# Kernel tuning notes

Hardware: AMD Instinct MI355X
Metric: run time of the kernel (lower is better)

## Reference

```python
import math
import jax, jax.numpy as jnp
import numpy as np

N_HEAD = 16
BLOCK_SIZE = 2048


def setup_inputs() -> dict:
    key = jax.random.key(0)
    ks = jax.random.split(key, 6)
    B, L, D = 2, 2048, 1024
    hs = D // N_HEAD
    s = 0.02
    return {
        "x": jax.random.normal(ks[0], (B, L, D), dtype=jnp.float32),
        "Wqkv": jax.random.normal(ks[1], (D, 3 * D), dtype=jnp.float32) * s,
        "bqkv": jax.random.normal(ks[2], (3 * D,), dtype=jnp.float32) * s,
        "Wproj": jax.random.normal(ks[3], (D, D), dtype=jnp.float32) * s,
        "bproj": jax.random.normal(ks[4], (D,), dtype=jnp.float32) * s,
        "Er": jax.random.normal(ks[5], (BLOCK_SIZE, hs), dtype=jnp.float32),
    }


def _skew(QEr):
    # QEr: [B, H, L, L] -> pad one zero column on the left, reshape, drop first row
    B, H, R, C = QEr.shape
    padded = jnp.pad(QEr, ((0, 0), (0, 0), (0, 0), (1, 0)))  # [B,H,R,C+1]
    reshaped = padded.reshape(B, H, C + 1, R)
    return reshaped[:, :, 1:, :]  # [B,H,R,C]


def reference(x, Wqkv, bqkv, Wproj, bproj, Er):
    B, L, D = x.shape
    H = N_HEAD
    hs = D // H
    qkv = x @ Wqkv + bqkv  # [B,L,3D]
    q, k, v = jnp.split(qkv, 3, axis=-1)
    q = q.reshape(B, L, H, hs).transpose(0, 2, 1, 3)  # [B,H,L,hs]
    k = k.reshape(B, L, H, hs).transpose(0, 2, 1, 3)
    v = v.reshape(B, L, H, hs).transpose(0, 2, 1, 3)

    Er_used = Er[BLOCK_SIZE - L:, :]           # [L, hs]
    QEr = jnp.einsum('bhld,md->bhlm', q, Er_used)  # q @ Er^T -> [B,H,L,L]
    Srel = _skew(QEr)

    scale = 1.0 / math.sqrt(hs)
    att = (jnp.einsum('bhld,bhmd->bhlm', q, k) + Srel) * scale
    causal = jnp.tril(jnp.ones((L, L), dtype=bool))
    att = jnp.where(causal[None, None], att, -jnp.inf)
    att = jax.nn.softmax(att, axis=-1)
    y = jnp.einsum('bhlm,bhmd->bhld', att, v)  # [B,H,L,hs]
    y = y.transpose(0, 2, 1, 3).reshape(B, L, D)
    return y @ Wproj + bproj
```

## Files before the change

kernel.cpp:

```cpp
#include <hip/hip_runtime.h>
#include <hip/hip_bf16.h>

#define LSEQ 2048
#define NH 16
#define HS 64
#define DIM 1024

typedef __attribute__((ext_vector_type(8))) short short8;
typedef __attribute__((ext_vector_type(4))) float f32x4;

typedef const __attribute__((address_space(1))) void g_void_t;
typedef __attribute__((address_space(3))) void s_void_t;

#define QSCALE 0.18033688011112042f

static __device__ __forceinline__ short f2bf(float f) {
  __hip_bfloat16 h = __float2bfloat16(f);
  return __builtin_bit_cast(short, h);
}

static __device__ __forceinline__ float fexp2(float x) {
#if __has_builtin(__builtin_amdgcn_exp2f)
  return __builtin_amdgcn_exp2f(x);
#else
  float r; asm("v_exp_f32 %0, %1" : "=v"(r) : "v"(x)); return r;
#endif
}

template<int CTRL>
static __device__ __forceinline__ float dpp_mov(float x) {
  return __builtin_bit_cast(float,
      __builtin_amdgcn_update_dpp(0, __builtin_bit_cast(int, x), CTRL, 0xF, 0xF, true));
}
static __device__ __forceinline__ float redmax16(float x) {
  x = fmaxf(x, dpp_mov<0xB1>(x));
  x = fmaxf(x, dpp_mov<0x4E>(x));
  x = fmaxf(x, dpp_mov<0x141>(x));
  x = fmaxf(x, dpp_mov<0x140>(x));
  return x;
}
static __device__ __forceinline__ float redsum16(float x) {
  x += dpp_mov<0xB1>(x);
  x += dpp_mov<0x4E>(x);
  x += dpp_mov<0x141>(x);
  x += dpp_mov<0x140>(x);
  return x;
}


__global__ void cast_kernel(const float* __restrict__ in, short* __restrict__ out, int n4) {
  int i = blockIdx.x * blockDim.x + threadIdx.x;
  if (i < n4) {
    float4 v = reinterpret_cast<const float4*>(in)[i];
    short4 o;
    o.x = f2bf(v.x); o.y = f2bf(v.y); o.z = f2bf(v.z); o.w = f2bf(v.w);
    reinterpret_cast<short4*>(out)[i] = o;
  }
}

__global__ void transpose_cast_kernel(const float* __restrict__ W, short* __restrict__ Wt,
                                      int K, int N) {
  __shared__ float tile[64][65];
  int k0 = blockIdx.y * 64, n0 = blockIdx.x * 64;
  int t = threadIdx.x;
  int r4 = t >> 6, cc = t & 63;
  for (int i = 0; i < 16; ++i) {
    int row = i * 4 + r4;
    tile[row][cc] = W[(size_t)(k0 + row) * N + (n0 + cc)];
  }
  __syncthreads();
  for (int i = 0; i < 16; ++i) {
    int row = i * 4 + r4;
    Wt[(size_t)(n0 + row) * K + (k0 + cc)] = f2bf(tile[cc][row]);
  }
}

__global__ void transpose_v_kernel(const short* __restrict__ V, short* __restrict__ Vt) {
  __shared__ short tile[64][65];
  int bh = blockIdx.y;
  int l0 = blockIdx.x * 64;
  int t = threadIdx.x;
  const short* src = V + ((size_t)bh * LSEQ + l0) * HS;
  for (int i = 0; i < 2; ++i) {
    int ch = i * 256 + t;
    int row = ch >> 3, c8 = ch & 7;
    uint4 v = *reinterpret_cast<const uint4*>(src + row * HS + c8 * 8);
    short tmp[8];
    *reinterpret_cast<uint4*>(tmp) = v;
#pragma unroll
    for (int e = 0; e < 8; ++e) tile[row][c8 * 8 + e] = tmp[e];
  }
  __syncthreads();
  short* dst = Vt + (size_t)bh * HS * LSEQ + l0;
  for (int i = 0; i < 2; ++i) {
    int ch = i * 256 + t;
    int d = ch >> 3, c8 = ch & 7;
    short tmp[8];
#pragma unroll
    for (int e = 0; e < 8; ++e) tmp[e] = tile[c8 * 8 + e][d];
    *reinterpret_cast<uint4*>(dst + (size_t)d * LSEQ + c8 * 8) = *reinterpret_cast<uint4*>(tmp);
  }
}


template<int MODE>
__global__ __launch_bounds__(256, 2) void gemm_bt_kernel(
    const short* __restrict__ A, const short* __restrict__ Bt,
    const float* __restrict__ bias, int M, int N, int K,
    short* __restrict__ oq, short* __restrict__ ok, short* __restrict__ ov,
    float* __restrict__ of)
{
  __shared__ short Al[128 * 32];
  __shared__ short Bl[128 * 32];
  const int m0 = blockIdx.y * 128, n0 = blockIdx.x * 128;
  const int t = threadIdx.x;
  const int lane = t & 63, wave = t >> 6;
  const int wr = wave >> 1, wc = wave & 1;
  const int g = lane >> 4, c = lane & 15;
  f32x4 acc[4][4] = {};

  for (int k0 = 0; k0 < K; k0 += 32) {
    __syncthreads();
    for (int i = 0; i < 2; ++i) {
      int ch = i * 256 + t;
      int row = ch >> 2, c8 = ch & 3;
      __builtin_amdgcn_global_load_lds(
          (g_void_t*)(A + (size_t)(m0 + row) * K + k0 + c8 * 8),
          (s_void_t*)(Al + (i * 256 + wave * 64) * 8), 16, 0, 0);
      __builtin_amdgcn_global_load_lds(
          (g_void_t*)(Bt + (size_t)(n0 + row) * K + k0 + c8 * 8),
          (s_void_t*)(Bl + (i * 256 + wave * 64) * 8), 16, 0, 0);
    }
    __syncthreads();
    short8 af[4], bf[4];
#pragma unroll
    for (int mi = 0; mi < 4; ++mi) {
      int row = wr * 64 + mi * 16 + c;
      af[mi] = *reinterpret_cast<const short8*>(Al + row * 32 + g * 8);
    }
#pragma unroll
    for (int ni = 0; ni < 4; ++ni) {
      int row = wc * 64 + ni * 16 + c;
      bf[ni] = *reinterpret_cast<const short8*>(Bl + row * 32 + g * 8);
    }
#pragma unroll
    for (int mi = 0; mi < 4; ++mi)
#pragma unroll
      for (int ni = 0; ni < 4; ++ni)
        acc[mi][ni] = __builtin_amdgcn_mfma_f32_16x16x32_bf16(af[mi], bf[ni], acc[mi][ni], 0, 0, 0);
  }

#pragma unroll
  for (int mi = 0; mi < 4; ++mi)
#pragma unroll
    for (int ni = 0; ni < 4; ++ni) {
      int n = n0 + wc * 64 + ni * 16 + c;
      float bv = bias[n];
#pragma unroll
      for (int r = 0; r < 4; ++r) {
        int m = m0 + wr * 64 + mi * 16 + g * 4 + r;
        float val = acc[mi][ni][r] + bv;
        if (MODE == 0) {
          int which = n >> 10;
          int hh2 = (n >> 6) & 15;
          int d = n & 63;
          int b = m >> 11, ll = m & 2047;
          if (which == 0) val *= QSCALE;
          short* dst = which == 0 ? oq : (which == 1 ? ok : ov);
          dst[(((size_t)b * NH + hh2) * LSEQ + ll) * HS + d] = f2bf(val);
        } else {
          of[(size_t)m * N + n] = val;
        }
      }
    }
}


__global__ __launch_bounds__(256, 2) void attn_kernel(
    const short* __restrict__ Qb, const short* __restrict__ Kb,
    const short* __restrict__ VTb, const short* __restrict__ Erb,
    short* __restrict__ Y)
{
  const int bid = blockIdx.x;
  const int pair = bid >> 5;
  const int bh = bid & 31;
  const int bb = bh >> 4, hh = bh & 15;
  const int t = threadIdx.x;
  const int lane = t & 63, wave = t >> 6;
  const int g = lane >> 4, c = lane & 15;
  const int r8 = lane >> 3;
  const int c16b = (lane & 7) * 16;

  __shared__ short Ql[64 * 64];
  __shared__ short Kl[2][64 * 64];
  __shared__ short Vl[2][64 * 64];
  __shared__ short El[2][128 * 64];
  __shared__ short Pl[4][16 * 64];

  auto process = [&](int qt) {
    const int l0 = qt * 64;

    const short* Qg = Qb + ((size_t)bh * LSEQ + l0) * HS;
    for (int i = 0; i < 2; ++i) {
      int ch = i * 256 + t;
      int row = ch >> 3, c8 = ch & 7;
      uint4 v = *reinterpret_cast<const uint4*>(Qg + row * HS + c8 * 8);
      int byte = row * 128 + ((c8 * 16) ^ ((row & 7) << 4));
      *reinterpret_cast<uint4*>(reinterpret_cast<char*>(Ql) + byte) = v;
    }
    __syncthreads();

    short8 qf[2];
#pragma unroll
    for (int kk = 0; kk < 2; ++kk) {
      int row = wave * 16 + c;
      int byte = row * 128 + ((kk * 32 + g * 8) * 2 ^ ((row & 7) << 4));
      qf[kk] = *reinterpret_cast<const short8*>(reinterpret_cast<char*>(Ql) + byte);
    }

    f32x4 acc_o[4] = {};
    float mrun[4], lrun[4];
#pragma unroll
    for (int r = 0; r < 4; ++r) { mrun[r] = -1e30f; lrun[r] = 0.0f; }

    const int nsteps = qt + 1;

    auto issue_stage = [&](int step, int sel) {
      const int m0 = step * 64;
      const char* Kg = (const char*)(Kb + ((size_t)bh * LSEQ + m0) * HS);
#pragma unroll
      for (int j = 0; j < 2; ++j) {
        int row = wave * 16 + j * 8 + r8;
        __builtin_amdgcn_global_load_lds(
            (g_void_t*)(Kg + row * 128 + (c16b ^ ((row & 7) << 4))),
            (s_void_t*)(&Kl[sel][(wave * 16 + j * 8) * 64]), 16, 0, 0);
      }
#pragma unroll
      for (int j = 0; j < 2; ++j) {
        int row = wave * 16 + j * 8 + r8;
        const char* Vg = (const char*)(VTb + ((size_t)bh * HS + row) * LSEQ + m0);
        __builtin_amdgcn_global_load_lds(
            (g_void_t*)(Vg + (c16b ^ ((row & 7) << 4))),
            (s_void_t*)(&Vl[sel][(wave * 16 + j * 8) * 64]), 16, 0, 0);
      }
      const int c0 = LSEQ - 1 - l0 + m0;
#pragma unroll
      for (int j = 0; j < 4; ++j) {
        int row = wave * 32 + j * 8 + r8;
        int e = c0 - 63 + row;
        e = e < 0 ? 0 : (e > LSEQ - 1 ? LSEQ - 1 : e);
        __builtin_amdgcn_global_load_lds(
            (g_void_t*)((const char*)(Erb + (size_t)e * HS) + (c16b ^ ((row & 7) << 4))),
            (s_void_t*)(&El[sel][(wave * 32 + j * 8) * 64]), 16, 0, 0);
      }
    };

    issue_stage(0, 0);

    for (int step = 0; step < nsteps; ++step) {
      const int sel = step & 1;
      const bool diag = (step == qt);

      if (step + 1 < nsteps) {
        issue_stage(step + 1, sel ^ 1);
        asm volatile("s_waitcnt vmcnt(8)" ::: "memory");
      } else {
        asm volatile("s_waitcnt vmcnt(0)" ::: "memory");
      }
      __builtin_amdgcn_s_barrier();
      __builtin_amdgcn_sched_barrier(0);

      f32x4 ga[5];
#pragma unroll
      for (int s5 = 0; s5 < 5; ++s5) {
        int nsb = (3 - wave) + s5;
        ga[s5] = (f32x4){0.0f, 0.0f, 0.0f, 0.0f};
#pragma unroll
        for (int kk = 0; kk < 2; ++kk) {
          int row = nsb * 16 + c;
          int byte = row * 128 + ((kk * 32 + g * 8) * 2 ^ ((row & 7) << 4));
          short8 ef = *reinterpret_cast<const short8*>((char*)El[sel] + byte);
          ga[s5] = __builtin_amdgcn_mfma_f32_16x16x32_bf16(qf[kk], ef, ga[s5], 0, 0, 0);
        }
      }

      f32x4 sa[4];
#pragma unroll
      for (int ns = 0; ns < 4; ++ns) {
        sa[ns] = (f32x4){0.0f, 0.0f, 0.0f, 0.0f};
#pragma unroll
        for (int kk = 0; kk < 2; ++kk) {
          int row = ns * 16 + c;
          int byte = row * 128 + ((kk * 32 + g * 8) * 2 ^ ((row & 7) << 4));
          short8 kf = *reinterpret_cast<const short8*>((char*)Kl[sel] + byte);
          sa[ns] = __builtin_amdgcn_mfma_f32_16x16x32_bf16(qf[kk], kf, sa[ns], 0, 0, 0);
        }
      }

      float sv[4][4];
#pragma unroll
      for (int r = 0; r < 4; ++r) {
        int i4 = g * 4 + r;
        int u0 = c + 15 - i4;
        int srcl = (g << 4) | (u0 & 15);
        float bp[5];
#pragma unroll
        for (int s5 = 0; s5 < 5; ++s5) bp[s5] = __shfl(ga[s5][r], srcl, 64);
        bool lo = (u0 < 16);
#pragma unroll
        for (int ns = 0; ns < 4; ++ns) {
          float srel = lo ? bp[ns] : bp[ns + 1];
          float x = sa[ns][r] + srel;
          if (diag && (ns * 16 + c > wave * 16 + i4)) x = -1e30f;
          sv[ns][r] = x;
        }
      }

      float mx[4];
      bool need = false;
#pragma unroll
      for (int r = 0; r < 4; ++r) {
        float m = fmaxf(fmaxf(sv[0][r], sv[1][r]), fmaxf(sv[2][r], sv[3][r]));
        mx[r] = redmax16(m);
        need = need || (mx[r] > mrun[r] + 4.0f);
      }
      if (__ballot(need)) {
#pragma unroll
        for (int r = 0; r < 4; ++r) {
          float mnew = fmaxf(mrun[r], mx[r]);
          float al = fexp2(mrun[r] - mnew);
          mrun[r] = mnew;
          lrun[r] *= al;
#pragma unroll
          for (int ns = 0; ns < 4; ++ns) acc_o[ns][r] *= al;
        }
      }
#pragma unroll
      for (int ns = 0; ns < 4; ++ns)
#pragma unroll
        for (int r = 0; r < 4; ++r)
          sv[ns][r] = fexp2(sv[ns][r] - mrun[r]);
#pragma unroll
      for (int r = 0; r < 4; ++r) {
        float s = (sv[0][r] + sv[1][r]) + (sv[2][r] + sv[3][r]);
        lrun[r] += redsum16(s);
      }

      short* Pw = Pl[wave];
#pragma unroll
      for (int ns = 0; ns < 4; ++ns)
#pragma unroll
        for (int r = 0; r < 4; ++r) {
          int row = g * 4 + r;
          int byte = row * 128 + (((ns * 16 + c) * 2) ^ ((row & 7) << 4));
          *reinterpret_cast<short*>(reinterpret_cast<char*>(Pw) + byte) = f2bf(sv[ns][r]);
        }

#pragma unroll
      for (int kk = 0; kk < 2; ++kk) {
        int kbyte = (kk * 32 + g * 8) * 2;
        int byteP = c * 128 + (kbyte ^ ((c & 7) << 4));
        short8 pf = *reinterpret_cast<const short8*>(reinterpret_cast<char*>(Pw) + byteP);
#pragma unroll
        for (int ns = 0; ns < 4; ++ns) {
          int rowV = ns * 16 + c;
          int byteV = rowV * 128 + (kbyte ^ ((rowV & 7) << 4));
          short8 vf = *reinterpret_cast<const short8*>((char*)Vl[sel] + byteV);
          acc_o[ns] = __builtin_amdgcn_mfma_f32_16x16x32_bf16(pf, vf, acc_o[ns], 0, 0, 0);
        }
      }

      __builtin_amdgcn_sched_barrier(0);
      __builtin_amdgcn_s_barrier();
    }

#pragma unroll
    for (int ns = 0; ns < 4; ++ns)
#pragma unroll
      for (int r = 0; r < 4; ++r) {
        int row = g * 4 + r;
        float inv = 1.0f / lrun[r];
        int lg = l0 + wave * 16 + row;
        int d = ns * 16 + c;
        Y[((size_t)bb * LSEQ + lg) * DIM + hh * HS + d] = f2bf(acc_o[ns][r] * inv);
      }
  };

  process(31 - pair);
  process(pair);
}


extern "C" void kernel_launch(void* const* d_in, const int* in_sizes, int n_in,
                              void* d_out, int out_size, void* d_ws, size_t ws_size,
                              hipStream_t stream)
{
  const float* x     = (const float*)d_in[0];
  const float* Wqkv  = (const float*)d_in[1];
  const float* bqkv  = (const float*)d_in[2];
  const float* Wproj = (const float*)d_in[3];
  const float* bproj = (const float*)d_in[4];
  const float* Er    = (const float*)d_in[5];

  char* ws = (char*)d_ws;
  short* xb     = (short*)(ws + 0);
  short* WqkvT  = (short*)(ws + 8388608);
  short* WprojT = (short*)(ws + 14680064);
  short* Erb    = (short*)(ws + 16777216);
  short* qB     = (short*)(ws + 17039360);
  short* kB     = (short*)(ws + 25427968);
  short* vB     = (short*)(ws + 33816576);
  short* yB     = (short*)(ws + 42205184);
  short* vT     = xb;

  cast_kernel<<<4096, 256, 0, stream>>>(x, xb, 4096 * 1024 / 4);
  cast_kernel<<<128, 256, 0, stream>>>(Er, Erb, 2048 * 64 / 4);
  transpose_cast_kernel<<<dim3(3072 / 64, 1024 / 64), 256, 0, stream>>>(Wqkv, WqkvT, 1024, 3072);
  transpose_cast_kernel<<<dim3(1024 / 64, 1024 / 64), 256, 0, stream>>>(Wproj, WprojT, 1024, 1024);

  gemm_bt_kernel<0><<<dim3(3072 / 128, 4096 / 128), 256, 0, stream>>>(
      xb, WqkvT, bqkv, 4096, 3072, 1024, qB, kB, vB, nullptr);

  transpose_v_kernel<<<dim3(32, 32), 256, 0, stream>>>(vB, vT);

  attn_kernel<<<dim3(512), 256, 0, stream>>>(qB, kB, vT, Erb, yB);

  gemm_bt_kernel<1><<<dim3(1024 / 128, 4096 / 128), 256, 0, stream>>>(
      yB, WprojT, bproj, 4096, 1024, 1024, nullptr, nullptr, nullptr, (float*)d_out);
}
```

Before: 153.2 us.

## Process adjacent query tiles jointly sharing K/V/Er loads; fuse prep kernels

The attention kernel now handles two adjacent query tiles (2p, 2p+1) in one pass, so the K, V and Er tiles staged to LDS serve both. Er is kept in a 4-slot ring of 64-row chunks, so only one new chunk is fetched per step instead of 128 rows. Q fragments are read straight from global memory into registers without an LDS staging step. The four cast and transpose prep launches are merged into a single kernel to save launch overhead. In exchange, the block pairing changes load balance (pairs of similar length instead of long plus short), register pressure rises from two sets of accumulators, and each step waits for vmcnt(0) instead of overlapping loads more deeply.

```diff
diff --git a/kernel.cpp b/kernel.cpp
--- a/kernel.cpp
+++ b/kernel.cpp
@@ -48,20 +48,29 @@
 }
 
 
-__global__ void cast_kernel(const float* __restrict__ in, short* __restrict__ out, int n4) {
-  int i = blockIdx.x * blockDim.x + threadIdx.x;
-  if (i < n4) {
+__global__ void prep_kernel(const float* __restrict__ x, const float* __restrict__ Er,
+                            const float* __restrict__ Wqkv, const float* __restrict__ Wproj,
+                            short* __restrict__ xb, short* __restrict__ Erb,
+                            short* __restrict__ WqkvT, short* __restrict__ WprojT) {
+  __shared__ float tile[64][65];
+  int bid = blockIdx.x;
+  if (bid < 4224) {
+    const float* in; short* out; int i0;
+    if (bid < 4096) { in = x;  out = xb;  i0 = bid * 256; }
+    else            { in = Er; out = Erb; i0 = (bid - 4096) * 256; }
+    int i = i0 + threadIdx.x;
     float4 v = reinterpret_cast<const float4*>(in)[i];
     short4 o;
     o.x = f2bf(v.x); o.y = f2bf(v.y); o.z = f2bf(v.z); o.w = f2bf(v.w);
     reinterpret_cast<short4*>(out)[i] = o;
-  }
-}
-
-__global__ void transpose_cast_kernel(const float* __restrict__ W, short* __restrict__ Wt,
-                                      int K, int N) {
-  __shared__ float tile[64][65];
-  int k0 = blockIdx.y * 64, n0 = blockIdx.x * 64;
+    return;
+  }
+  int id = bid - 4224;
+  const float* W; short* Wt; int N, tx, ty;
+  if (id < 768) { W = Wqkv;  Wt = WqkvT;  N = 3072; tx = id % 48; ty = id / 48; }
+  else { id -= 768; W = Wproj; Wt = WprojT; N = 1024; tx = id % 16; ty = id / 16; }
+  const int K = 1024;
+  int k0 = ty * 64, n0 = tx * 64;
   int t = threadIdx.x;
   int r4 = t >> 6, cc = t & 63;
   for (int i = 0; i < 16; ++i) {
@@ -182,8 +191,11 @@
     short* __restrict__ Y)
 {
   const int bid = blockIdx.x;
-  const int pair = bid >> 5;
+  const int p = 15 - (bid >> 5);
   const int bh = bid & 31;
+  const int qtH = 2 * p + 1, qtL = 2 * p;
+  const int l0H = qtH * 64, l0L = qtL * 64;
+  const int nbase = 30 - 2 * p;
   const int bb = bh >> 4, hh = bh & 15;
   const int t = threadIdx.x;
   const int lane = t & 63, wave = t >> 6;
@@ -191,203 +203,204 @@
   const int r8 = lane >> 3;
   const int c16b = (lane & 7) * 16;
 
-  __shared__ short Ql[64 * 64];
-  __shared__ short Kl[2][64 * 64];
+  __shared__ short Kl[64 * 64];
   __shared__ short Vl[2][64 * 64];
-  __shared__ short El[2][128 * 64];
+  __shared__ short El[4][64 * 64];
   __shared__ short Pl[4][16 * 64];
 
-  auto process = [&](int qt) {
-    const int l0 = qt * 64;
-
-    const short* Qg = Qb + ((size_t)bh * LSEQ + l0) * HS;
-    for (int i = 0; i < 2; ++i) {
-      int ch = i * 256 + t;
-      int row = ch >> 3, c8 = ch & 7;
-      uint4 v = *reinterpret_cast<const uint4*>(Qg + row * HS + c8 * 8);
-      int byte = row * 128 + ((c8 * 16) ^ ((row & 7) << 4));
-      *reinterpret_cast<uint4*>(reinterpret_cast<char*>(Ql) + byte) = v;
-    }
-    __syncthreads();
-
-    short8 qf[2];
-#pragma unroll
-    for (int kk = 0; kk < 2; ++kk) {
-      int row = wave * 16 + c;
-      int byte = row * 128 + ((kk * 32 + g * 8) * 2 ^ ((row & 7) << 4));
-      qf[kk] = *reinterpret_cast<const short8*>(reinterpret_cast<char*>(Ql) + byte);
-    }
-
-    f32x4 acc_o[4] = {};
-    float mrun[4], lrun[4];
-#pragma unroll
-    for (int r = 0; r < 4; ++r) { mrun[r] = -1e30f; lrun[r] = 0.0f; }
-
-    const int nsteps = qt + 1;
-
-    auto issue_stage = [&](int step, int sel) {
-      const int m0 = step * 64;
-      const char* Kg = (const char*)(Kb + ((size_t)bh * LSEQ + m0) * HS);
-#pragma unroll
-      for (int j = 0; j < 2; ++j) {
-        int row = wave * 16 + j * 8 + r8;
-        __builtin_amdgcn_global_load_lds(
-            (g_void_t*)(Kg + row * 128 + (c16b ^ ((row & 7) << 4))),
-            (s_void_t*)(&Kl[sel][(wave * 16 + j * 8) * 64]), 16, 0, 0);
-      }
-#pragma unroll
-      for (int j = 0; j < 2; ++j) {
-        int row = wave * 16 + j * 8 + r8;
-        const char* Vg = (const char*)(VTb + ((size_t)bh * HS + row) * LSEQ + m0);
-        __builtin_amdgcn_global_load_lds(
-            (g_void_t*)(Vg + (c16b ^ ((row & 7) << 4))),
-            (s_void_t*)(&Vl[sel][(wave * 16 + j * 8) * 64]), 16, 0, 0);
-      }
-      const int c0 = LSEQ - 1 - l0 + m0;
-#pragma unroll
-      for (int j = 0; j < 4; ++j) {
-        int row = wave * 32 + j * 8 + r8;
-        int e = c0 - 63 + row;
-        e = e < 0 ? 0 : (e > LSEQ - 1 ? LSEQ - 1 : e);
-        __builtin_amdgcn_global_load_lds(
-            (g_void_t*)((const char*)(Erb + (size_t)e * HS) + (c16b ^ ((row & 7) << 4))),
-            (s_void_t*)(&El[sel][(wave * 32 + j * 8) * 64]), 16, 0, 0);
-      }
-    };
-
-    issue_stage(0, 0);
-
-    for (int step = 0; step < nsteps; ++step) {
-      const int sel = step & 1;
-      const bool diag = (step == qt);
-
-      if (step + 1 < nsteps) {
-        issue_stage(step + 1, sel ^ 1);
-        asm volatile("s_waitcnt vmcnt(8)" ::: "memory");
-      } else {
-        asm volatile("s_waitcnt vmcnt(0)" ::: "memory");
-      }
-      __builtin_amdgcn_s_barrier();
-      __builtin_amdgcn_sched_barrier(0);
-
-      f32x4 ga[5];
-#pragma unroll
-      for (int s5 = 0; s5 < 5; ++s5) {
-        int nsb = (3 - wave) + s5;
-        ga[s5] = (f32x4){0.0f, 0.0f, 0.0f, 0.0f};
-#pragma unroll
-        for (int kk = 0; kk < 2; ++kk) {
-          int row = nsb * 16 + c;
-          int byte = row * 128 + ((kk * 32 + g * 8) * 2 ^ ((row & 7) << 4));
-          short8 ef = *reinterpret_cast<const short8*>((char*)El[sel] + byte);
-          ga[s5] = __builtin_amdgcn_mfma_f32_16x16x32_bf16(qf[kk], ef, ga[s5], 0, 0, 0);
-        }
-      }
-
-      f32x4 sa[4];
+  const short* QgH = Qb + ((size_t)bh * LSEQ + l0H) * HS;
+  const short* QgL = Qb + ((size_t)bh * LSEQ + l0L) * HS;
+  short8 qfH[2], qfL[2];
+#pragma unroll
+  for (int kk = 0; kk < 2; ++kk) {
+    qfH[kk] = *reinterpret_cast<const short8*>(QgH + (wave * 16 + c) * HS + kk * 32 + g * 8);
+    qfL[kk] = *reinterpret_cast<const short8*>(QgL + (wave * 16 + c) * HS + kk * 32 + g * 8);
+  }
+
+  auto stage_K = [&](int step) {
+    const char* Kg = (const char*)(Kb + ((size_t)bh * LSEQ + step * 64) * HS);
+#pragma unroll
+    for (int j = 0; j < 2; ++j) {
+      int row = wave * 16 + j * 8 + r8;
+      __builtin_amdgcn_global_load_lds(
+          (g_void_t*)(Kg + row * 128 + (c16b ^ ((row & 7) << 4))),
+          (s_void_t*)(&Kl[(wave * 16 + j * 8) * 64]), 16, 0, 0);
+    }
+  };
+  auto stage_V = [&](int step) {
+    int sel = step & 1;
+#pragma unroll
+    for (int j = 0; j < 2; ++j) {
+      int row = wave * 16 + j * 8 + r8;
+      const char* Vg = (const char*)(VTb + ((size_t)bh * HS + row) * LSEQ + step * 64);
+      __builtin_amdgcn_global_load_lds(
+          (g_void_t*)(Vg + (c16b ^ ((row & 7) << 4))),
+          (s_void_t*)(&Vl[sel][(wave * 16 + j * 8) * 64]), 16, 0, 0);
+    }
+  };
+  auto stage_E = [&](int chunk) {
+    int slot = chunk & 3;
+#pragma unroll
+    for (int j = 0; j < 2; ++j) {
+      int row = wave * 16 + j * 8 + r8;
+      int e = chunk * 64 + row;
+      if (e > LSEQ - 1) e = LSEQ - 1;
+      __builtin_amdgcn_global_load_lds(
+          (g_void_t*)((const char*)Erb + (size_t)e * 128 + (c16b ^ ((row & 7) << 4))),
+          (s_void_t*)(&El[slot][(wave * 16 + j * 8) * 64]), 16, 0, 0);
+    }
+  };
+
+  auto gs = [&](const short8* qf, int nT, f32x4* ga, f32x4* sa) {
+#pragma unroll
+    for (int s5 = 0; s5 < 5; ++s5) {
+      int nsb = (3 - wave) + s5;
+      int rb = nsb * 16 + c;
+      int ch = nT + (rb >> 6);
+      int phys = ((ch & 3) << 6) | (rb & 63);
+      ga[s5] = (f32x4){0.0f, 0.0f, 0.0f, 0.0f};
+#pragma unroll
+      for (int kk = 0; kk < 2; ++kk) {
+        int byte = phys * 128 + (((kk * 32 + g * 8) * 2) ^ ((rb & 7) << 4));
+        short8 ef = *reinterpret_cast<const short8*>((char*)El + byte);
+        ga[s5] = __builtin_amdgcn_mfma_f32_16x16x32_bf16(qf[kk], ef, ga[s5], 0, 0, 0);
+      }
+    }
+#pragma unroll
+    for (int ns = 0; ns < 4; ++ns) {
+      sa[ns] = (f32x4){0.0f, 0.0f, 0.0f, 0.0f};
+#pragma unroll
+      for (int kk = 0; kk < 2; ++kk) {
+        int row = ns * 16 + c;
+        int byte = row * 128 + (((kk * 32 + g * 8) * 2) ^ ((row & 7) << 4));
+        short8 kf = *reinterpret_cast<const short8*>((char*)Kl + byte);
+        sa[ns] = __builtin_amdgcn_mfma_f32_16x16x32_bf16(qf[kk], kf, sa[ns], 0, 0, 0);
+      }
+    }
+  };
+
+  auto post = [&](f32x4* ga, f32x4* sa, bool diag, int selV,
+                  f32x4* acc_o, float* mrun, float* lrun) {
+    float sv[4][4];
+#pragma unroll
+    for (int r = 0; r < 4; ++r) {
+      int i4 = g * 4 + r;
+      int u0 = c + 15 - i4;
+      int srcl = (g << 4) | (u0 & 15);
+      float bp[5];
+#pragma unroll
+      for (int s5 = 0; s5 < 5; ++s5) bp[s5] = __shfl(ga[s5][r], srcl, 64);
+      bool lo = (u0 < 16);
 #pragma unroll
       for (int ns = 0; ns < 4; ++ns) {
-        sa[ns] = (f32x4){0.0f, 0.0f, 0.0f, 0.0f};
-#pragma unroll
-        for (int kk = 0; kk < 2; ++kk) {
-          int row = ns * 16 + c;
-          int byte = row * 128 + ((kk * 32 + g * 8) * 2 ^ ((row & 7) << 4));
-          short8 kf = *reinterpret_cast<const short8*>((char*)Kl[sel] + byte);
-          sa[ns] = __builtin_amdgcn_mfma_f32_16x16x32_bf16(qf[kk], kf, sa[ns], 0, 0, 0);
-        }
-      }
-
-      float sv[4][4];
+        float srel = lo ? bp[ns] : bp[ns + 1];
+        float xx = sa[ns][r] + srel;
+        if (diag && (ns * 16 + c > wave * 16 + i4)) xx = -1e30f;
+        sv[ns][r] = xx;
+      }
+    }
+
+    float mx[4];
+    bool need = false;
+#pragma unroll
+    for (int r = 0; r < 4; ++r) {
+      float m = fmaxf(fmaxf(sv[0][r], sv[1][r]), fmaxf(sv[2][r], sv[3][r]));
+      mx[r] = redmax16(m);
+      need = need || (mx[r] > mrun[r] + 4.0f);
+    }
+    if (__ballot(need)) {
 #pragma unroll
       for (int r = 0; r < 4; ++r) {
-        int i4 = g * 4 + r;
-        int u0 = c + 15 - i4;
-        int srcl = (g << 4) | (u0 & 15);
-        float bp[5];
-#pragma unroll
-        for (int s5 = 0; s5 < 5; ++s5) bp[s5] = __shfl(ga[s5][r], srcl, 64);
-        bool lo = (u0 < 16);
-#pragma unroll
-        for (int ns = 0; ns < 4; ++ns) {
-          float srel = lo ? bp[ns] : bp[ns + 1];
-          float x = sa[ns][r] + srel;
-          if (diag && (ns * 16 + c > wave * 16 + i4)) x = -1e30f;
-          sv[ns][r] = x;
-        }
-      }
-
-      float mx[4];
-      bool need = false;
-#pragma unroll
-      for (int r = 0; r < 4; ++r) {
-        float m = fmaxf(fmaxf(sv[0][r], sv[1][r]), fmaxf(sv[2][r], sv[3][r]));
-        mx[r] = redmax16(m);
-        need = need || (mx[r] > mrun[r] + 4.0f);
-      }
-      if (__ballot(need)) {
-#pragma unroll
-        for (int r = 0; r < 4; ++r) {
-          float mnew = fmaxf(mrun[r], mx[r]);
-          float al = fexp2(mrun[r] - mnew);
-          mrun[r] = mnew;
-          lrun[r] *= al;
-#pragma unroll
-          for (int ns = 0; ns < 4; ++ns) acc_o[ns][r] *= al;
-        }
-      }
-#pragma unroll
-      for (int ns = 0; ns < 4; ++ns)
-#pragma unroll
-        for (int r = 0; r < 4; ++r)
-          sv[ns][r] = fexp2(sv[ns][r] - mrun[r]);
-#pragma unroll
-      for (int r = 0; r < 4; ++r) {
-        float s = (sv[0][r] + sv[1][r]) + (sv[2][r] + sv[3][r]);
-        lrun[r] += redsum16(s);
-      }
-
-      short* Pw = Pl[wave];
-#pragma unroll
-      for (int ns = 0; ns < 4; ++ns)
-#pragma unroll
-        for (int r = 0; r < 4; ++r) {
-          int row = g * 4 + r;
-          int byte = row * 128 + (((ns * 16 + c) * 2) ^ ((row & 7) << 4));
-          *reinterpret_cast<short*>(reinterpret_cast<char*>(Pw) + byte) = f2bf(sv[ns][r]);
-        }
-
-#pragma unroll
-      for (int kk = 0; kk < 2; ++kk) {
-        int kbyte = (kk * 32 + g * 8) * 2;
-        int byteP = c * 128 + (kbyte ^ ((c & 7) << 4));
-        short8 pf = *reinterpret_cast<const short8*>(reinterpret_cast<char*>(Pw) + byteP);
-#pragma unroll
-        for (int ns = 0; ns < 4; ++ns) {
-          int rowV = ns * 16 + c;
-          int byteV = rowV * 128 + (kbyte ^ ((rowV & 7) << 4));
-          short8 vf = *reinterpret_cast<const short8*>((char*)Vl[sel] + byteV);
-          acc_o[ns] = __builtin_amdgcn_mfma_f32_16x16x32_bf16(pf, vf, acc_o[ns], 0, 0, 0);
-        }
-      }
-
-      __builtin_amdgcn_sched_barrier(0);
-      __builtin_amdgcn_s_barrier();
-    }
-
+        float mnew = fmaxf(mrun[r], mx[r]);
+        float al = fexp2(mrun[r] - mnew);
+        mrun[r] = mnew;
+        lrun[r] *= al;
+#pragma unroll
+        for (int ns = 0; ns < 4; ++ns) acc_o[ns][r] *= al;
+      }
+    }
+#pragma unroll
+    for (int ns = 0; ns < 4; ++ns)
+#pragma unroll
+      for (int r = 0; r < 4; ++r)
+        sv[ns][r] = fexp2(sv[ns][r] - mrun[r]);
+#pragma unroll
+    for (int r = 0; r < 4; ++r) {
+      float s = (sv[0][r] + sv[1][r]) + (sv[2][r] + sv[3][r]);
+      lrun[r] += redsum16(s);
+    }
+
+    short* Pw = Pl[wave];
 #pragma unroll
     for (int ns = 0; ns < 4; ++ns)
 #pragma unroll
       for (int r = 0; r < 4; ++r) {
         int row = g * 4 + r;
-        float inv = 1.0f / lrun[r];
-        int lg = l0 + wave * 16 + row;
-        int d = ns * 16 + c;
-        Y[((size_t)bb * LSEQ + lg) * DIM + hh * HS + d] = f2bf(acc_o[ns][r] * inv);
-      }
+        int byte = row * 128 + (((ns * 16 + c) * 2) ^ ((row & 7) << 4));
+        *reinterpret_cast<short*>(reinterpret_cast<char*>(Pw) + byte) = f2bf(sv[ns][r]);
+      }
+#pragma unroll
+    for (int kk = 0; kk < 2; ++kk) {
+      int kbyte = (kk * 32 + g * 8) * 2;
+      int byteP = c * 128 + (kbyte ^ ((c & 7) << 4));
+      short8 pf = *reinterpret_cast<const short8*>(reinterpret_cast<char*>(Pw) + byteP);
+#pragma unroll
+      for (int ns = 0; ns < 4; ++ns) {
+        int rowV = ns * 16 + c;
+        int byteV = rowV * 128 + (kbyte ^ ((rowV & 7) << 4));
+        short8 vf = *reinterpret_cast<const short8*>((char*)Vl[selV] + byteV);
+        acc_o[ns] = __builtin_amdgcn_mfma_f32_16x16x32_bf16(pf, vf, acc_o[ns], 0, 0, 0);
+      }
+    }
   };
 
-  process(31 - pair);
-  process(pair);
+  stage_V(0);
+  stage_K(0);
+  stage_E(nbase); stage_E(nbase + 1); stage_E(nbase + 2);
+
+  f32x4 accH[4] = {}, accL[4] = {};
+  float mH[4], lH[4], mL[4], lL[4];
+#pragma unroll
+  for (int r = 0; r < 4; ++r) { mH[r] = -1e30f; lH[r] = 0.0f; mL[r] = -1e30f; lL[r] = 0.0f; }
+
+  for (int s = 0; s <= qtH; ++s) {
+    const int sel = s & 1;
+    const bool doL = (s <= qtL);
+    const int nH = nbase + s;
+
+    asm volatile("s_waitcnt vmcnt(0)" ::: "memory");
+    __builtin_amdgcn_s_barrier();
+    __builtin_amdgcn_sched_barrier(0);
+
+    f32x4 gaH[5], saH[4], gaL[5], saL[4];
+    gs(qfH, nH, gaH, saH);
+    if (doL) gs(qfL, nH + 1, gaL, saL);
+
+    __builtin_amdgcn_sched_barrier(0);
+    __builtin_amdgcn_s_barrier();
+    __builtin_amdgcn_sched_barrier(0);
+
+    if (s < qtH) {
+      stage_V(s + 1);
+      stage_K(s + 1);
+      stage_E(nbase + s + 3);
+    }
+
+    post(gaH, saH, s == qtH, sel, accH, mH, lH);
+    if (doL) post(gaL, saL, s == qtL, sel, accL, mL, lL);
+  }
+
+#pragma unroll
+  for (int ns = 0; ns < 4; ++ns)
+#pragma unroll
+    for (int r = 0; r < 4; ++r) {
+      int row = g * 4 + r;
+      int d = ns * 16 + c;
+      int lgH = l0H + wave * 16 + row;
+      Y[((size_t)bb * LSEQ + lgH) * DIM + hh * HS + d] = f2bf(accH[ns][r] / lH[r]);
+      int lgL = l0L + wave * 16 + row;
+      Y[((size_t)bb * LSEQ + lgL) * DIM + hh * HS + d] = f2bf(accL[ns][r] / lL[r]);
+    }
 }
 
 
@@ -413,10 +426,7 @@
   short* yB     = (short*)(ws + 42205184);
   short* vT     = xb;
 
-  cast_kernel<<<4096, 256, 0, stream>>>(x, xb, 4096 * 1024 / 4);
-  cast_kernel<<<128, 256, 0, stream>>>(Er, Erb, 2048 * 64 / 4);
-  transpose_cast_kernel<<<dim3(3072 / 64, 1024 / 64), 256, 0, stream>>>(Wqkv, WqkvT, 1024, 3072);
-  transpose_cast_kernel<<<dim3(1024 / 64, 1024 / 64), 256, 0, stream>>>(Wproj, WprojT, 1024, 1024);
+  prep_kernel<<<dim3(5248), 256, 0, stream>>>(x, Er, Wqkv, Wproj, xb, Erb, WqkvT, WprojT);
 
   gemm_bt_kernel<0><<<dim3(3072 / 128, 4096 / 128), 256, 0, stream>>>(
       xb, WqkvT, bqkv, 4096, 3072, 1024, qB, kB, vB, nullptr);
```

Result: slower. 170.1 us (+11.1%).
